# Kernel tuning notes

Hardware: AMD Instinct MI355X
Metric: run time of the kernel (lower is better)

## Reference

```python
import jax, jax.numpy as jnp
import numpy as np

B, E, H, OUT, T = 256, 256, 256, 702, 512


def setup_inputs() -> dict:
    key = jax.random.key(0)
    ks = jax.random.split(key, 7)
    s = 1.0 / np.sqrt(H)  # PyTorch LSTM init scale
    return {
        "embed": jax.random.normal(ks[0], (B, 1, E), jnp.float32),
        "W_ih": jax.random.normal(ks[1], (4 * H, E), jnp.float32) * s,
        "W_hh": jax.random.normal(ks[2], (4 * H, H), jnp.float32) * s,
        "b_ih": jax.random.normal(ks[3], (4 * H,), jnp.float32) * s,
        "b_hh": jax.random.normal(ks[4], (4 * H,), jnp.float32) * s,
        "W_rec": jax.random.normal(ks[5], (OUT, H), jnp.float32) * s,
        "b_rec": jax.random.normal(ks[6], (OUT,), jnp.float32) * s,
        "sequence_length": T,
    }


def reference(embed, W_ih, W_hh, b_ih, b_hh, W_rec, b_rec, sequence_length):
    # embed: [B, 1, E]; decoder_type == 3 -> next input = out + embed
    x0 = embed[:, 0, :]  # [B, E]
    batch = x0.shape[0]
    hdim = W_hh.shape[1]

    def step(carry, _):
        h, c, x = carry
        gates = x @ W_ih.T + b_ih + h @ W_hh.T + b_hh  # [B, 4H]
        i, f, g, o = jnp.split(gates, 4, axis=-1)  # PyTorch gate order i,f,g,o
        c = jax.nn.sigmoid(f) * c + jax.nn.sigmoid(i) * jnp.tanh(g)
        h = jax.nn.sigmoid(o) * jnp.tanh(c)
        x_next = h + x0  # decoder_type 3 feedback
        return (h, c, x_next), h

    h0 = jnp.zeros((batch, hdim), embed.dtype)
    c0 = jnp.zeros((batch, hdim), embed.dtype)
    _, hs = jax.lax.scan(step, (h0, c0, x0), None, length=sequence_length)
    sequence_decoded = jnp.transpose(hs, (1, 0, 2))  # [B, T, H]
    sequence_reconstructed = sequence_decoded @ W_rec.T + b_rec  # [B, T, 702]
    return sequence_reconstructed, sequence_decoded
```

## Files before the change

kernel.cpp:

```cpp
#include <hip/hip_runtime.h>
#include <hip/hip_bf16.h>

#define B_   256
#define E_   256
#define H_   256
#define T_   512
#define OUT_ 702
#define G4H  1024

typedef _Float16 half8 __attribute__((ext_vector_type(8)));
typedef float    floatx4 __attribute__((ext_vector_type(4)));
typedef unsigned long long ull;

#define OFF_DTF    0
#define OFF_HBUF   4096
#define OFF_BASE   (4096 + 524288)
#define OFF_WC16   (OFF_BASE + 1048576)
#define OFF_WREC16 (OFF_WC16 + 524288)
#define OFF_HS16   (OFF_WREC16 + 360448)

__device__ __forceinline__ float ldin(const void* p, long i, int bf) {
  return bf ? __bfloat162float(((const __hip_bfloat16*)p)[i]) : ((const float*)p)[i];
}
__device__ __forceinline__ void stout(void* p, long i, float v, int bf) {
  if (bf) ((__hip_bfloat16*)p)[i] = __float2bfloat16(v);
  else    ((float*)p)[i] = v;
}
__device__ __forceinline__ float sigf(float x)  { return 1.0f / (1.0f + __expf(-x)); }
__device__ __forceinline__ float tanh_(float x) { float e = __expf(2.0f * x); return 1.0f - 2.0f / (e + 1.0f); }

__global__ void k_detect(const unsigned int* emb, int* dtf) {
  int tid = threadIdx.x;
  int cnt = 0;
  for (int i = tid; i < 256; i += 64) {
    unsigned int u = emb[i];
    unsigned int e = (u >> 7) & 0xFF;
    cnt += (e >= 100 && e <= 129) ? 1 : 0;
  }
  for (int off = 32; off > 0; off >>= 1) cnt += __shfl_down(cnt, off);
  if (tid == 0) *dtf = (cnt >= 128) ? 1 : 0;
}

__global__ void k_prep_wc(const void* wih, const void* whh, _Float16* wc, const int* dtf) {
  int bf = *dtf;
  long i = (long)blockIdx.x * 256 + threadIdx.x;
  wc[i] = (_Float16)(ldin(wih, i, bf) + ldin(whh, i, bf));
}

__global__ void k_prep_wrec(const void* wrec, _Float16* wr, const int* dtf) {
  int bf = *dtf;
  long i = (long)blockIdx.x * 256 + threadIdx.x;
  wr[i] = (i < (long)OUT_ * H_) ? (_Float16)ldin(wrec, i, bf) : (_Float16)0.0f;
}

__global__ void k_prep_base(const void* emb, const void* wih, const void* bih,
                            const void* bhh, float* base, const int* dtf) {
  int bf = *dtf;
  int b = blockIdx.x >> 2;
  int n = (blockIdx.x & 3) * 256 + threadIdx.x;
  __shared__ float x0s[256];
  x0s[threadIdx.x] = ldin(emb, (long)b * E_ + threadIdx.x, bf);
  __syncthreads();
  float acc = ldin(bih, n, bf) + ldin(bhh, n, bf);
  const long wrow = (long)n * E_;
  for (int k = 0; k < E_; ++k) acc += x0s[k] * ldin(wih, wrow + k, bf);
  base[(long)b * G4H + n] = acc;
}

__global__ void __launch_bounds__(256) k_lstm(char* ws, void* dout, const int* dtf) {
  const int bf  = *dtf;
  const int tid = threadIdx.x;
  const int g   = blockIdx.x >> 4;
  const int mem = blockIdx.x & 15;
  const int wid = tid >> 6;
  const int lane = tid & 63;
  const int q = lane >> 4;
  const int r = lane & 15;
  const int gid = r >> 2;
  const int cl  = r & 3;

  _Float16* wc   = (_Float16*)(ws + OFF_WC16);
  float*    base = (float*)(ws + OFF_BASE);
  ull*      hbuf = (ull*)(ws + OFF_HBUF);
  _Float16* hs16 = (_Float16*)(ws + OFF_HS16);

  const int mycol = mem * 16 + wid * 4 + cl;
  const int myrow = q * 4 + gid;

  half8 wfrag[8];
  {
    const long wrow = (long)(gid * 256 + mycol) * H_;
#pragma unroll
    for (int kb = 0; kb < 8; ++kb)
      wfrag[kb] = *(const half8*)(wc + wrow + kb * 32 + q * 8);
  }
  float basev[4];
  {
    const long brow = (long)(g * 16 + myrow) * G4H + mycol;
#pragma unroll
    for (int G = 0; G < 4; ++G) basev[G] = base[brow + G * 256];
  }

  __shared__ _Float16 h_lds[2][16][264];
  for (int i = tid; i < 2 * 16 * 264; i += 256) (&h_lds[0][0][0])[i] = (_Float16)0.0f;
  float c = 0.0f;
  __syncthreads();

  const long out2off = (long)B_ * T_ * OUT_;
  const long orow_base = ((long)(g * 16 + myrow) * T_) * H_ + mycol;

  const bool packer = (cl == 0);
  const int pword = (g * 16 + myrow) * 64 + mem * 4 + wid;
  const int grow = g * 16 + wid * 4;

  int cur = 0;
  for (int t = 0; t < T_; ++t) {
    floatx4 acc = {0.f, 0.f, 0.f, 0.f};
#pragma unroll
    for (int kb = 0; kb < 8; ++kb) {
      half8 a = *(const half8*)(&h_lds[cur][r][kb * 32 + q * 8]);
      acc = __builtin_amdgcn_mfma_f32_16x16x32_f16(a, wfrag[kb], acc, 0, 0, 0);
    }
    float a0 = acc[0], a1 = acc[1], a2 = acc[2], a3 = acc[3];
    float own = gid == 0 ? a0 : gid == 1 ? a1 : gid == 2 ? a2 : a3;
    float vi = own, vf = own, vg = own, vo = own;
#pragma unroll
    for (int cc = 1; cc < 4; ++cc) {
      int sg = (gid + cc) & 3;
      float sv = sg == 0 ? a0 : sg == 1 ? a1 : sg == 2 ? a2 : a3;
      int src = (lane & 48) + (((gid - cc) & 3) << 2) + cl;
      float rv = __shfl(sv, src);
      int rg = (gid - cc) & 3;
      vi = (rg == 0) ? rv : vi;
      vf = (rg == 1) ? rv : vf;
      vg = (rg == 2) ? rv : vg;
      vo = (rg == 3) ? rv : vo;
    }
    float giv = vi + basev[0];
    float gfv = vf + basev[1];
    float ggv = vg + basev[2];
    float gov = vo + basev[3];
    c = sigf(gfv) * c + sigf(giv) * tanh_(ggv);
    float h = sigf(gov) * tanh_(c);

    if (t < T_ - 1) {
      const int slot = t & 3;
      union { _Float16 f; unsigned short u; } cv; cv.f = (_Float16)h;
      unsigned int hu = cv.u;
      const int lb = lane & ~3;
      unsigned int u0 = __shfl(hu, lb);
      unsigned int u1 = __shfl(hu, lb + 1);
      unsigned int u2 = __shfl(hu, lb + 2);
      unsigned int u3 = __shfl(hu, lb + 3);
      if (packer) {
        if (t >= 2)
          __hip_atomic_store(&hbuf[((long)((t - 2) & 3) << 14) + pword], 0ULL,
                             __ATOMIC_RELAXED, __HIP_MEMORY_SCOPE_AGENT);
        ull w = (ull)(u0 & 0xFFFFu)
              | ((ull)(u1 & 0xFFFFu) << 16)
              | ((ull)(u2 & 0xFFFFu) << 32)
              | ((ull)(u3 & 0xFFFFu) << 48);
        __hip_atomic_store(&hbuf[((long)slot << 14) + pword], ~w,
                           __ATOMIC_RELAXED, __HIP_MEMORY_SCOPE_AGENT);
      }

      stout(dout, out2off + orow_base + (long)t * H_, h, bf);
      hs16[orow_base + (long)t * H_] = (_Float16)h;

      const ull* sb = hbuf + ((long)slot << 14);
      ull d[4] = {0, 0, 0, 0};
      unsigned int pend = 0xFu;
      int guard = 0;
      while (pend) {
        const unsigned int snap = pend;
        ull tmp[4];
#pragma unroll
        for (int i = 0; i < 4; ++i)
          if (snap & (1u << i))
            tmp[i] = __hip_atomic_load(&sb[(long)(grow + i) * 64 + lane],
                                       __ATOMIC_RELAXED, __HIP_MEMORY_SCOPE_AGENT);
#pragma unroll
        for (int i = 0; i < 4; ++i)
          if (snap & (1u << i)) {
            if (tmp[i]) { d[i] = ~tmp[i]; pend &= ~(1u << i); }
          }
        ++guard;
        if (guard > 64) __builtin_amdgcn_s_sleep(1);
        if (guard > 500000) break;
      }
      asm volatile("s_waitcnt vmcnt(0)" ::: "memory");
      const int nxt = cur ^ 1;
#pragma unroll
      for (int i = 0; i < 4; ++i)
        *(ull*)(&h_lds[nxt][wid * 4 + i][lane * 4]) = d[i];
      __syncthreads();
      cur = nxt;
    } else {
      stout(dout, out2off + orow_base + (long)t * H_, h, bf);
      hs16[orow_base + (long)t * H_] = (_Float16)h;
    }
  }
}

__global__ void __launch_bounds__(256) k_proj(const char* ws, const void* brec,
                                              void* dout, const int* dtf) {
  const int bf  = *dtf;
  const int tid = threadIdx.x;
  const int wid = tid >> 6, lane = tid & 63, q = lane >> 4, r = lane & 15;
  const int mb = blockIdx.x & 2047, nb = blockIdx.x >> 11;
  const long mbase = (long)mb * 64;
  const int  nbase = nb * 192;
  const _Float16* hs16 = (const _Float16*)(ws + OFF_HS16);
  const _Float16* wr16 = (const _Float16*)(ws + OFF_WREC16);

  __shared__ _Float16 a_lds[64][264];
#pragma unroll
  for (int i = 0; i < 8; ++i) {
    int u = tid + i * 256;
    int row = u >> 5, c8 = (u & 31) * 8;
    half8 v = *(const half8*)(hs16 + (mbase + row) * H_ + c8);
    *(half8*)(&a_lds[row][c8]) = v;
  }
  __syncthreads();

  half8 bfrag[3][8];
  float bias[3];
#pragma unroll
  for (int j = 0; j < 3; ++j) {
    int ncol = nbase + (wid * 3 + j) * 16 + r;
    bias[j] = 0.0f;
    if (ncol < 704) {
      const long wrow = (long)ncol * H_;
#pragma unroll
      for (int kb = 0; kb < 8; ++kb)
        bfrag[j][kb] = *(const half8*)(wr16 + wrow + kb * 32 + q * 8);
    } else {
      half8 z = {0, 0, 0, 0, 0, 0, 0, 0};
#pragma unroll
      for (int kb = 0; kb < 8; ++kb) bfrag[j][kb] = z;
    }
    if (ncol < OUT_) bias[j] = ldin(brec, ncol, bf);
  }

  floatx4 acc[3][4];
#pragma unroll
  for (int j = 0; j < 3; ++j)
#pragma unroll
    for (int ms = 0; ms < 4; ++ms) acc[j][ms] = (floatx4){0.f, 0.f, 0.f, 0.f};

#pragma unroll
  for (int ms = 0; ms < 4; ++ms) {
#pragma unroll
    for (int kb = 0; kb < 8; ++kb) {
      half8 a = *(const half8*)(&a_lds[ms * 16 + r][kb * 32 + q * 8]);
#pragma unroll
      for (int j = 0; j < 3; ++j)
        acc[j][ms] = __builtin_amdgcn_mfma_f32_16x16x32_f16(a, bfrag[j][kb], acc[j][ms], 0, 0, 0);
    }
  }

#pragma unroll
  for (int j = 0; j < 3; ++j) {
    int ncol = nbase + (wid * 3 + j) * 16 + r;
    if (ncol >= OUT_) continue;
#pragma unroll
    for (int ms = 0; ms < 4; ++ms) {
#pragma unroll
      for (int e = 0; e < 4; ++e) {
        long mrow = mbase + ms * 16 + q * 4 + e;
        stout(dout, mrow * (long)OUT_ + ncol, acc[j][ms][e] + bias[j], bf);
      }
    }
  }
}

extern "C" void kernel_launch(void* const* d_in, const int* in_sizes, int n_in,
                              void* d_out, int out_size, void* d_ws, size_t ws_size,
                              hipStream_t stream) {
  const void* embed = d_in[0];
  const void* W_ih  = d_in[1];
  const void* W_hh  = d_in[2];
  const void* b_ih  = d_in[3];
  const void* b_hh  = d_in[4];
  const void* W_rec = d_in[5];
  const void* b_rec = d_in[6];
  char* ws = (char*)d_ws;
  const int* dtf = (const int*)(ws + OFF_DTF);

  hipMemsetAsync(ws, 0, OFF_BASE, stream);
  k_detect<<<1, 64, 0, stream>>>((const unsigned int*)embed, (int*)(ws + OFF_DTF));
  k_prep_wc<<<1024, 256, 0, stream>>>(W_ih, W_hh, (_Float16*)(ws + OFF_WC16), dtf);
  k_prep_wrec<<<704, 256, 0, stream>>>(W_rec, (_Float16*)(ws + OFF_WREC16), dtf);
  k_prep_base<<<1024, 256, 0, stream>>>(embed, W_ih, b_ih, b_hh, (float*)(ws + OFF_BASE), dtf);
  k_lstm<<<256, 256, 0, stream>>>(ws, d_out, dtf);
  k_proj<<<8192, 256, 0, stream>>>(ws, b_rec, d_out, dtf);
}
```

Before: 1.711 ms.

## Coalesce LSTM hidden-state stores from LDS and enlarge projection M tiles

The LSTM kernel no longer has each lane write its own scattered h element to the decoded output and the fp16 buffer. It writes the previous step's h row from the LDS exchange buffer with coalesced row-wise stores, one step late, and adds a tail store after the loop. The projection kernel doubles its M tile to 128 rows with an XOR-swizzled 64KB LDS layout and half as many blocks, so each W_rec fragment is reused more. The cost is higher LDS and register use per block, which may lower occupancy.

```diff
diff --git a/kernel.cpp b/kernel.cpp
--- a/kernel.cpp
+++ b/kernel.cpp
@@ -106,8 +106,8 @@
   float c = 0.0f;
   __syncthreads();
 
-  const long out2off = (long)B_ * T_ * OUT_;
-  const long orow_base = ((long)(g * 16 + myrow) * T_) * H_ + mycol;
+  const long obase  = (long)B_ * T_ * OUT_ + ((long)(g * 16 + mem) * T_) * H_;
+  _Float16* hsrow = hs16 + ((long)(g * 16 + mem) * T_) * H_;
 
   const bool packer = (cl == 0);
   const int pword = (g * 16 + myrow) * 64 + mem * 4 + wid;
@@ -143,83 +143,98 @@
     c = sigf(gfv) * c + sigf(giv) * tanh_(ggv);
     float h = sigf(gov) * tanh_(c);
 
-    if (t < T_ - 1) {
-      const int slot = t & 3;
-      union { _Float16 f; unsigned short u; } cv; cv.f = (_Float16)h;
-      unsigned int hu = cv.u;
-      const int lb = lane & ~3;
-      unsigned int u0 = __shfl(hu, lb);
-      unsigned int u1 = __shfl(hu, lb + 1);
-      unsigned int u2 = __shfl(hu, lb + 2);
-      unsigned int u3 = __shfl(hu, lb + 3);
-      if (packer) {
-        if (t >= 2)
-          __hip_atomic_store(&hbuf[((long)((t - 2) & 3) << 14) + pword], 0ULL,
-                             __ATOMIC_RELAXED, __HIP_MEMORY_SCOPE_AGENT);
-        ull w = (ull)(u0 & 0xFFFFu)
-              | ((ull)(u1 & 0xFFFFu) << 16)
-              | ((ull)(u2 & 0xFFFFu) << 32)
-              | ((ull)(u3 & 0xFFFFu) << 48);
-        __hip_atomic_store(&hbuf[((long)slot << 14) + pword], ~w,
+    const int slot = t & 3;
+    union { _Float16 f; unsigned short u; } cv; cv.f = (_Float16)h;
+    unsigned int hu = cv.u;
+    const int lb = lane & ~3;
+    unsigned int u0 = __shfl(hu, lb);
+    unsigned int u1 = __shfl(hu, lb + 1);
+    unsigned int u2 = __shfl(hu, lb + 2);
+    unsigned int u3 = __shfl(hu, lb + 3);
+    if (packer) {
+      if (t >= 2)
+        __hip_atomic_store(&hbuf[((long)((t - 2) & 3) << 14) + pword], 0ULL,
                            __ATOMIC_RELAXED, __HIP_MEMORY_SCOPE_AGENT);
+      ull w = (ull)(u0 & 0xFFFFu)
+            | ((ull)(u1 & 0xFFFFu) << 16)
+            | ((ull)(u2 & 0xFFFFu) << 32)
+            | ((ull)(u3 & 0xFFFFu) << 48);
+      __hip_atomic_store(&hbuf[((long)slot << 14) + pword], ~w,
+                         __ATOMIC_RELAXED, __HIP_MEMORY_SCOPE_AGENT);
+    }
+
+    if (t > 0) {
+      const long o = obase + (long)(t - 1) * H_;
+      float hv = (float)h_lds[cur][mem][tid];
+      stout(dout, o + tid, hv, bf);
+      if (wid == 0) {
+        ull v = *(const ull*)(&h_lds[cur][mem][lane * 4]);
+        *(ull*)(hsrow + (long)(t - 1) * H_ + lane * 4) = v;
       }
-
-      stout(dout, out2off + orow_base + (long)t * H_, h, bf);
-      hs16[orow_base + (long)t * H_] = (_Float16)h;
-
-      const ull* sb = hbuf + ((long)slot << 14);
-      ull d[4] = {0, 0, 0, 0};
-      unsigned int pend = 0xFu;
-      int guard = 0;
-      while (pend) {
-        const unsigned int snap = pend;
-        ull tmp[4];
-#pragma unroll
-        for (int i = 0; i < 4; ++i)
-          if (snap & (1u << i))
-            tmp[i] = __hip_atomic_load(&sb[(long)(grow + i) * 64 + lane],
-                                       __ATOMIC_RELAXED, __HIP_MEMORY_SCOPE_AGENT);
-#pragma unroll
-        for (int i = 0; i < 4; ++i)
-          if (snap & (1u << i)) {
-            if (tmp[i]) { d[i] = ~tmp[i]; pend &= ~(1u << i); }
-          }
-        ++guard;
-        if (guard > 64) __builtin_amdgcn_s_sleep(1);
-        if (guard > 500000) break;
-      }
-      asm volatile("s_waitcnt vmcnt(0)" ::: "memory");
-      const int nxt = cur ^ 1;
+    }
+
+    const ull* sb = hbuf + ((long)slot << 14);
+    ull d[4] = {0, 0, 0, 0};
+    unsigned int pend = 0xFu;
+    int guard = 0;
+    while (pend) {
+      const unsigned int snap = pend;
+      ull tmp[4];
 #pragma unroll
       for (int i = 0; i < 4; ++i)
-        *(ull*)(&h_lds[nxt][wid * 4 + i][lane * 4]) = d[i];
-      __syncthreads();
-      cur = nxt;
-    } else {
-      stout(dout, out2off + orow_base + (long)t * H_, h, bf);
-      hs16[orow_base + (long)t * H_] = (_Float16)h;
-    }
-  }
-}
-
+        if (snap & (1u << i))
+          tmp[i] = __hip_atomic_load(&sb[(long)(grow + i) * 64 + lane],
+                                     __ATOMIC_RELAXED, __HIP_MEMORY_SCOPE_AGENT);
+#pragma unroll
+      for (int i = 0; i < 4; ++i)
+        if (snap & (1u << i)) {
+          if (tmp[i]) { d[i] = ~tmp[i]; pend &= ~(1u << i); }
+        }
+      ++guard;
+      if (guard > 64) __builtin_amdgcn_s_sleep(1);
+      if (guard > 500000) break;
+    }
+    asm volatile("s_waitcnt vmcnt(0)" ::: "memory");
+    const int nxt = cur ^ 1;
+#pragma unroll
+    for (int i = 0; i < 4; ++i)
+      *(ull*)(&h_lds[nxt][wid * 4 + i][lane * 4]) = d[i];
+    __syncthreads();
+    cur = nxt;
+  }
+
+  {
+    const long o = obase + (long)(T_ - 1) * H_;
+    float hv = (float)h_lds[cur][mem][tid];
+    stout(dout, o + tid, hv, bf);
+    if (wid == 0) {
+      ull v = *(const ull*)(&h_lds[cur][mem][lane * 4]);
+      *(ull*)(hsrow + (long)(T_ - 1) * H_ + lane * 4) = v;
+    }
+  }
+}
+
+__device__ __forceinline__ int aswz(int row, int hc) {
+  return ((row << 9) + (hc << 1)) ^ ((row & 7) << 4);
+}
 __global__ void __launch_bounds__(256) k_proj(const char* ws, const void* brec,
                                               void* dout, const int* dtf) {
   const int bf  = *dtf;
   const int tid = threadIdx.x;
   const int wid = tid >> 6, lane = tid & 63, q = lane >> 4, r = lane & 15;
-  const int mb = blockIdx.x & 2047, nb = blockIdx.x >> 11;
-  const long mbase = (long)mb * 64;
+  const int mb = blockIdx.x >> 2, nb = blockIdx.x & 3;
+  const long mbase = (long)mb * 128;
   const int  nbase = nb * 192;
   const _Float16* hs16 = (const _Float16*)(ws + OFF_HS16);
   const _Float16* wr16 = (const _Float16*)(ws + OFF_WREC16);
 
-  __shared__ _Float16 a_lds[64][264];
-#pragma unroll
-  for (int i = 0; i < 8; ++i) {
+  __shared__ __align__(16) char a_raw[65536];
+#pragma unroll
+  for (int i = 0; i < 16; ++i) {
     int u = tid + i * 256;
     int row = u >> 5, c8 = (u & 31) * 8;
     half8 v = *(const half8*)(hs16 + (mbase + row) * H_ + c8);
-    *(half8*)(&a_lds[row][c8]) = v;
+    *(half8*)(a_raw + aswz(row, c8)) = v;
   }
   __syncthreads();
 
@@ -242,17 +257,17 @@
     if (ncol < OUT_) bias[j] = ldin(brec, ncol, bf);
   }
 
-  floatx4 acc[3][4];
+  floatx4 acc[3][8];
 #pragma unroll
   for (int j = 0; j < 3; ++j)
 #pragma unroll
-    for (int ms = 0; ms < 4; ++ms) acc[j][ms] = (floatx4){0.f, 0.f, 0.f, 0.f};
-
-#pragma unroll
-  for (int ms = 0; ms < 4; ++ms) {
+    for (int ms = 0; ms < 8; ++ms) acc[j][ms] = (floatx4){0.f, 0.f, 0.f, 0.f};
+
+#pragma unroll
+  for (int ms = 0; ms < 8; ++ms) {
 #pragma unroll
     for (int kb = 0; kb < 8; ++kb) {
-      half8 a = *(const half8*)(&a_lds[ms * 16 + r][kb * 32 + q * 8]);
+      half8 a = *(const half8*)(a_raw + aswz(ms * 16 + r, kb * 32 + q * 8));
 #pragma unroll
       for (int j = 0; j < 3; ++j)
         acc[j][ms] = __builtin_amdgcn_mfma_f32_16x16x32_f16(a, bfrag[j][kb], acc[j][ms], 0, 0, 0);
@@ -264,7 +279,7 @@
     int ncol = nbase + (wid * 3 + j) * 16 + r;
     if (ncol >= OUT_) continue;
 #pragma unroll
-    for (int ms = 0; ms < 4; ++ms) {
+    for (int ms = 0; ms < 8; ++ms) {
 #pragma unroll
       for (int e = 0; e < 4; ++e) {
         long mrow = mbase + ms * 16 + q * 4 + e;
@@ -293,5 +308,5 @@
   k_prep_wrec<<<704, 256, 0, stream>>>(W_rec, (_Float16*)(ws + OFF_WREC16), dtf);
   k_prep_base<<<1024, 256, 0, stream>>>(embed, W_ih, b_ih, b_hh, (float*)(ws + OFF_BASE), dtf);
   k_lstm<<<256, 256, 0, stream>>>(ws, d_out, dtf);
-  k_proj<<<8192, 256, 0, stream>>>(ws, b_rec, d_out, dtf);
-}
+  k_proj<<<4096, 256, 0, stream>>>(ws, b_rec, d_out, dtf);
+}
```

Measured after the change: 1.854 ms. 1.08x slower.
